# Kernel optimization log

Measured on AMD Instinct MI355X. Metric: run time of the kernel, lower is better.

## Reference

```python
import jax, jax.numpy as jnp
import numpy as np

H = 256; NHEAD = 2; DH = H // NHEAD; FF = NHEAD * H // 2
NODE_FEATS = [40, 8, 6]; EDGE_FEATS = [5, 4]; NIN = sum(NODE_FEATS)
S = 256; B = 4; NL_NODE = 2; NL_EDGE = 1
NEG = np.float32(-1e9)

# static edge-window bookkeeping: for i in 1..S-1, group i attends to nodes [max(0,i-12), i)
_idx = []; _grp = []
for _i in range(1, S):
    _st = max(0, _i - 12)
    _idx += list(range(_st, _i)); _grp += [_i] * (_i - _st)
IDX = np.asarray(_idx); GRP = np.asarray(_grp); LE = len(_idx)
MEM_MASK = np.full((LE, S + 1), NEG, np.float32)
MEM_MASK[:, 0] = 0.0; MEM_MASK[np.arange(LE), GRP + 1] = 0.0
EDGE_TGT_MASK = np.where(GRP[:, None] == GRP[None, :], np.float32(0.0), NEG)
CAUSAL = np.triu(np.full((S, S), NEG, np.float32), 1)
SIN_F = (1.0 / 10000.0 ** (np.arange(0, H, 2) / H)).astype(np.float32)
COS_F = (1.0 / 10000.0 ** (np.arange(1, H, 2) / H)).astype(np.float32)

def _ln(x, g, b):
    m = x.mean(-1, keepdims=True)
    v = ((x - m) ** 2).mean(-1, keepdims=True)
    return (x - m) / jnp.sqrt(v + 1e-5) * g + b

def _mha(q_in, kv_in, qkv_w, qkv_b, o_w, o_b, mask):
    Lq, Bb, _ = q_in.shape; Lk = kv_in.shape[0]
    wq, wk, wv = jnp.split(qkv_w, 3, 0); bq, bk, bv = jnp.split(qkv_b, 3, 0)
    q = (q_in @ wq.T + bq).reshape(Lq, Bb, NHEAD, DH)
    k = (kv_in @ wk.T + bk).reshape(Lk, Bb, NHEAD, DH)
    v = (kv_in @ wv.T + bv).reshape(Lk, Bb, NHEAD, DH)
    s = jnp.einsum('qbhd,kbhd->bhqk', q, k) * np.float32(1.0 / np.sqrt(DH))
    if mask is not None:
        s = s + mask
    p = jax.nn.softmax(s, -1)
    o = jnp.einsum('bhqk,kbhd->qbhd', p, v).reshape(Lq, Bb, H)
    return o @ o_w.T + o_b

def _decoder(tgt, mem, P, tgt_mask, mem_mask):
    qkv_w, qkv_b, so_w, so_b, cqkv_w, cqkv_b, co_w, co_b, f1w, f1b, f2w, f2b, lg, lb, fg, fb = P
    for l in range(qkv_w.shape[0]):
        tgt = _ln(tgt + _mha(tgt, tgt, qkv_w[l], qkv_b[l], so_w[l], so_b[l], tgt_mask), lg[l, 0], lb[l, 0])
        tgt = _ln(tgt + _mha(tgt, mem, cqkv_w[l], cqkv_b[l], co_w[l], co_b[l], mem_mask), lg[l, 1], lb[l, 1])
        ff = jax.nn.relu(tgt @ f1w[l].T + f1b[l]) @ f2w[l].T + f2b[l]
        tgt = _ln(tgt + ff, lg[l, 2], lb[l, 2])
    return _ln(tgt, fg, fb)

def _ce(logits, tgt):
    lp = jax.nn.log_softmax(logits, -1)
    nll = -jnp.take_along_axis(lp, jnp.clip(tgt, 0)[:, None], 1)[:, 0]
    valid = (tgt >= 0).astype(lp.dtype)
    return (nll * valid).sum() / jnp.maximum(valid.sum(), 1.0)

def _forward(z, atom_x, Wp, bp, bn_g, bn_b, ndP, edP, ncls, ecls, atom_i, atom_y, bond_y):
    x = atom_x.reshape(-1, NIN) @ Wp.T + bp
    m = x.mean(0); v2 = ((x - m) ** 2).mean(0)  # BatchNorm1d (training stats)
    x = jax.nn.selu((x - m) / jnp.sqrt(v2 + 1e-5) * bn_g + bn_b).reshape(S, B, H)
    pos = atom_i[..., 0].astype(jnp.float32)  # [S,B]
    pe = jnp.stack([jnp.sin(pos[:, :, None] * SIN_F), jnp.cos(pos[:, :, None] * COS_F)], -1).reshape(S, B, H)
    node_emb = _decoder(pe + x, z[None], ndP, CAUSAL, None)
    yt = atom_y.reshape(-1, atom_y.shape[-1])
    node_loss = 0.0
    for i, (w, b) in enumerate(ncls):
        node_loss = node_loss + _ce((node_emb @ w.T + b).reshape(-1, w.shape[0]), yt[:, i])
    edge_mem = jnp.concatenate([z[None], node_emb], 0)  # [S+1,B,H]
    edge_emb = _decoder(node_emb[IDX], edge_mem, edP, EDGE_TGT_MASK, MEM_MASK)
    et = bond_y.reshape(-1, bond_y.shape[-1])
    edge_loss = 0.0
    for i, (w, b) in enumerate(ecls):
        edge_loss = edge_loss + _ce((edge_emb @ w.T + b).reshape(-1, w.shape[0]), et[:, i])
    return node_loss + edge_loss

def setup_inputs():
    key = jax.random.key(0)
    cnt = [0]
    def nk():
        cnt[0] += 1
        return jax.random.fold_in(key, cnt[0])
    def rn(shape, s=0.05):
        return jax.random.normal(nk(), shape, jnp.float32) * s
    inp = {}
    inp['z'] = jax.random.normal(nk(), (B, H), jnp.float32)
    inp['atom_i'] = jax.random.randint(nk(), (S, B, 1), 0, S)
    inp['atom_x'] = jax.random.uniform(nk(), (S, B, NIN), dtype=jnp.float32)
    inp['atom_y'] = jax.random.randint(nk(), (S, B, 3), 0, 6)
    inp['bond_y'] = jax.random.randint(nk(), (LE, B, 2), 0, 4)
    inp['Wp'] = rn((H, NIN)); inp['bp'] = jnp.zeros((H,)); inp['bn_g'] = jnp.ones((H,)); inp['bn_b'] = jnp.zeros((H,))
    for pre, L in (('nd_', NL_NODE), ('ed_', NL_EDGE)):
        inp[pre + 'qkv_w'] = rn((L, 3 * H, H)); inp[pre + 'qkv_b'] = jnp.zeros((L, 3 * H))
        inp[pre + 'so_w'] = rn((L, H, H)); inp[pre + 'so_b'] = jnp.zeros((L, H))
        inp[pre + 'cqkv_w'] = rn((L, 3 * H, H)); inp[pre + 'cqkv_b'] = jnp.zeros((L, 3 * H))
        inp[pre + 'co_w'] = rn((L, H, H)); inp[pre + 'co_b'] = jnp.zeros((L, H))
        inp[pre + 'ff1_w'] = rn((L, FF, H)); inp[pre + 'ff1_b'] = jnp.zeros((L, FF))
        inp[pre + 'ff2_w'] = rn((L, H, FF)); inp[pre + 'ff2_b'] = jnp.zeros((L, H))
        inp[pre + 'ln_g'] = jnp.ones((L, 3, H)); inp[pre + 'ln_b'] = jnp.zeros((L, 3, H))
        inp[pre + 'fn_g'] = jnp.ones((H,)); inp[pre + 'fn_b'] = jnp.zeros((H,))
    for i, C in enumerate(NODE_FEATS):
        inp['nc%d_w' % i] = rn((C, H)); inp['nc%d_b' % i] = jnp.zeros((C,))
    for i, C in enumerate(EDGE_FEATS):
        inp['ec%d_w' % i] = rn((C, H)); inp['ec%d_b' % i] = jnp.zeros((C,))
    return inp

def reference(z, atom_i, atom_x, atom_y, bond_y, Wp, bp, bn_g, bn_b, nd_qkv_w, nd_qkv_b, nd_so_w, nd_so_b, nd_cqkv_w, nd_cqkv_b, nd_co_w, nd_co_b, nd_ff1_w, nd_ff1_b, nd_ff2_w, nd_ff2_b, nd_ln_g, nd_ln_b, nd_fn_g, nd_fn_b, ed_qkv_w, ed_qkv_b, ed_so_w, ed_so_b, ed_cqkv_w, ed_cqkv_b, ed_co_w, ed_co_b, ed_ff1_w, ed_ff1_b, ed_ff2_w, ed_ff2_b, ed_ln_g, ed_ln_b, ed_fn_g, ed_fn_b, nc0_w, nc0_b, nc1_w, nc1_b, nc2_w, nc2_b, ec0_w, ec0_b, ec1_w, ec1_b):
    ndP = (nd_qkv_w, nd_qkv_b, nd_so_w, nd_so_b, nd_cqkv_w, nd_cqkv_b, nd_co_w, nd_co_b, nd_ff1_w, nd_ff1_b, nd_ff2_w, nd_ff2_b, nd_ln_g, nd_ln_b, nd_fn_g, nd_fn_b)
    edP = (ed_qkv_w, ed_qkv_b, ed_so_w, ed_so_b, ed_cqkv_w, ed_cqkv_b, ed_co_w, ed_co_b, ed_ff1_w, ed_ff1_b, ed_ff2_w, ed_ff2_b, ed_ln_g, ed_ln_b, ed_fn_g, ed_fn_b)
    ncls = [(nc0_w, nc0_b), (nc1_w, nc1_b), (nc2_w, nc2_b)]
    ecls = [(ec0_w, ec0_b), (ec1_w, ec1_b)]
    return _forward(z, atom_x, Wp, bp, bn_g, bn_b, ndP, edP, ncls, ecls, atom_i, atom_y, bond_y)
```

## Files before the change

### kernel.cpp

```cpp
#include <hip/hip_runtime.h>
#include <math.h>

#define SS 256
#define BB 4
#define HH 256
#define LE 2994
#define LEB (LE*BB)
#define SCALE 0.08838834764831845f

typedef __attribute__((ext_vector_type(8))) short bf16x8;
typedef __attribute__((ext_vector_type(4))) float f32x4;

__device__ inline ushort f2b(float f) {
    unsigned u = __float_as_uint(f);
    u += 0x7FFFu + ((u >> 16) & 1u);
    return (ushort)(u >> 16);
}

__device__ inline float qred(float x) {
    x += __shfl_xor(x, 1); x += __shfl_xor(x, 2);
    x += __shfl_xor(x, 4); x += __shfl_xor(x, 8);
    return x;
}

// ... 232 lines not shown

__global__ __launch_bounds__(256) void k_node_mega(
    const float* __restrict__ t1, const float* __restrict__ tgt,
    const float* __restrict__ crO,
    const ushort* __restrict__ Wso, const float* __restrict__ so_b,
    const float* __restrict__ ln0g, const float* __restrict__ ln0b,
    const float* __restrict__ ln1g, const float* __restrict__ ln1b,
    const ushort* __restrict__ Wff1, const float* __restrict__ ff1_b,
    const ushort* __restrict__ Wff2, const float* __restrict__ ff2_b,
    const float* __restrict__ ln2g, const float* __restrict__ ln2b,
    const float* __restrict__ fng, const float* __restrict__ fnb,
    float* __restrict__ outp, int M, int finalln)
{
    __shared__ ushort As[8 * 512];
    __shared__ float red[128];
    int tid = threadIdx.x;
    int w = tid >> 6, lane = tid & 63, q = lane >> 4, p = lane & 15;
    int m0 = blockIdx.x * 16;

    float x[4][4];
    f32x4 acc[4];

    stageA_16(t1, M, m0, tid, As);
    #pragma unroll
    for (int reg = 0; reg < 4; reg++) {
        int row = m0 + q * 4 + reg;
        bool ok = row < M;
        #pragma unroll
        for (int nt = 0; nt < 4; nt++)
            x[nt][reg] = ok ? tgt[(size_t)row * 256 + w * 64 + nt * 16 + p] : 0.f;
    }

    gemm_pass16(As, Wso, w, lane, acc);
    {
        float bi[4];
        #pragma unroll
        for (int nt = 0; nt < 4; nt++) bi[nt] = so_b[w * 64 + nt * 16 + p];
        #pragma unroll
        for (int nt = 0; nt < 4; nt++)
            #pragma unroll
            for (int reg = 0; reg < 4; reg++)
                acc[nt][reg] += bi[nt] + x[nt][reg];
    }
    block_ln16(acc, red, tid, w, q, p, ln0g, ln0b);

    #pragma unroll
    for (int reg = 0; reg < 4; reg++) {
        int row = m0 + q * 4 + reg;
        int b = row & 3;
        #pragma unroll
        for (int nt = 0; nt < 4; nt++)
            acc[nt][reg] += crO[b * 256 + w * 64 + nt * 16 + p];
    }
    block_ln16(acc, red, tid, w, q, p, ln1g, ln1b);

    #pragma unroll
    for (int nt = 0; nt < 4; nt++)
        #pragma unroll
        for (int reg = 0; reg < 4; reg++)
            x[nt][reg] = acc[nt][reg];

    stage_acc16(acc, As, w, q, p);
    gemm_pass16(As, Wff1, w, lane, acc);
    {
        float bi[4];
        #pragma unroll
        for (int nt = 0; nt < 4; nt++) bi[nt] = ff1_b[w * 64 + nt * 16 + p];
        #pragma unroll
        for (int nt = 0; nt < 4; nt++)
            #pragma unroll
            for (int reg = 0; reg < 4; reg++)
                acc[nt][reg] = fmaxf(acc[nt][reg] + bi[nt], 0.f);
    }

    stage_acc16(acc, As, w, q, p);
    gemm_pass16(As, Wff2, w, lane, acc);
    {
        float bi[4];
        #pragma unroll
        for (int nt = 0; nt < 4; nt++) bi[nt] = ff2_b[w * 64 + nt * 16 + p];
        #pragma unroll
        for (int nt = 0; nt < 4; nt++)
            #pragma unroll
            for (int reg = 0; reg < 4; reg++)
                acc[nt][reg] += bi[nt] + x[nt][reg];
    }
    block_ln16(acc, red, tid, w, q, p, ln2g, ln2b);
    if (finalln) block_ln16(acc, red, tid, w, q, p, fng, fnb);

    #pragma unroll
    for (int reg = 0; reg < 4; reg++) {
        int row = m0 + q * 4 + reg;
        if (row >= M) continue;
        #pragma unroll
        for (int nt = 0; nt < 4; nt++)
            outp[(size_t)row * 256 + w * 64 + nt * 16 + p] = acc[nt][reg];
    }
}


__global__ __launch_bounds__(256) void k_edge_mega(
    const float* __restrict__ et1, const float* __restrict__ etgt,
    const ushort* __restrict__ Wso, const float* __restrict__ so_b,
    const float* __restrict__ ln0g, const float* __restrict__ ln0b,
    const ushort* __restrict__ Wcq, const float* __restrict__ cq_b,
    const float* __restrict__ KV, const int* __restrict__ grp,
    const ushort* __restrict__ Wco, const float* __restrict__ co_b,
    const float* __restrict__ ln1g, const float* __restrict__ ln1b,
    const ushort* __restrict__ Wff1, const float* __restrict__ ff1_b,
    const ushort* __restrict__ Wff2, const float* __restrict__ ff2_b,
    const float* __restrict__ ln2g, const float* __restrict__ ln2b,
    const float* __restrict__ fng, const float* __restrict__ fnb,
    const int* __restrict__ ydata,
    const float* __restrict__ cw0, const float* __restrict__ cb0,
    const float* __restrict__ cw1, const float* __restrict__ cb1,
    float* __restrict__ lossOut, float invM, int M)
{
    __shared__ ushort As[8 * 512];
    __shared__ float red[640];
    int tid = threadIdx.x;
    int w = tid >> 6, lane = tid & 63, q = lane >> 4, p = lane & 15;
    int m0 = blockIdx.x * 16;

    float x[4][4];
    f32x4 acc[4];

    stageA_16(et1, M, m0, tid, As);
    #pragma unroll
    for (int reg = 0; reg < 4; reg++) {
        int row = m0 + q * 4 + reg;
        bool ok = row < M;
        #pragma unroll
        for (int nt = 0; nt < 4; nt++)
            x[nt][reg] = ok ? etgt[(size_t)row * 256 + w * 64 + nt * 16 + p] : 0.f;
    }

    gemm_pass16(As, Wso, w, lane, acc);
    {
        float bi[4];
        #pragma unroll
        for (int nt = 0; nt < 4; nt++) bi[nt] = so_b[w * 64 + nt * 16 + p];
        #pragma unroll
        for (int nt = 0; nt < 4; nt++)
            #pragma unroll
            for (int reg = 0; reg < 4; reg++)
                acc[nt][reg] += bi[nt] + x[nt][reg];
    }
    block_ln16(acc, red, tid, w, q, p, ln0g, ln0b);
    #pragma unroll
    for (int nt = 0; nt < 4; nt++)
        #pragma unroll
        for (int reg = 0; reg < 4; reg++)
            x[nt][reg] = acc[nt][reg];

    stage_acc16(acc, As, w, q, p);
    gemm_pass16(As, Wcq, w, lane, acc);
    {
        int h = w >> 1;
        float bi[4];
        #pragma unroll
        for (int nt = 0; nt < 4; nt++) bi[nt] = cq_b[w * 64 + nt * 16 + p];
        #pragma unroll
        for (int reg = 0; reg < 4; reg++) {
            int lr = q * 4 + reg;
            int row = m0 + lr;
            bool ok = row < M;
            int b = row & 3;
            int g = ok ? grp[row >> 2] : 0;
            const float* K0 = KV + (size_t)b * 512 + h * 128;
            const float* K1 = KV + ((size_t)(g + 1) * 4 + b) * 512 + h * 128;
            float s0 = 0.f, s1 = 0.f;
            #pragma unroll
            for (int nt = 0; nt < 4; nt++) {
                float qv = acc[nt][reg] + bi[nt];
                int d = (w & 1) * 64 + nt * 16 + p;
                s0 += qv * K0[d]; s1 += qv * K1[d];
            }
            s0 = qred(s0); s1 = qred(s1);
            if (p == 0) { red[(w * 16 + lr) * 2 + 0] = s0; red[(w * 16 + lr) * 2 + 1] = s1; }
        }
        __syncthreads();
        if (tid < 32) {
            int hh = tid >> 4, lr = tid & 15;
            float p0 = (red[((hh * 2) * 16 + lr) * 2 + 0] + red[((hh * 2 + 1) * 16 + lr) * 2 + 0]) * SCALE;
            float p1 = (red[((hh * 2) * 16 + lr) * 2 + 1] + red[((hh * 2 + 1) * 16 + lr) * 2 + 1]) * SCALE;
            float mx = fmaxf(p0, p1);
            float e0 = __expf(p0 - mx), e1 = __expf(p1 - mx);
            float inv = 1.f / (e0 + e1);
            red[128 + (hh * 16 + lr) * 2 + 0] = e0 * inv;
            red[128 + (hh * 16 + lr) * 2 + 1] = e1 * inv;
        }
        __syncthreads();
        #pragma unroll
        for (int reg = 0; reg < 4; reg++) {
            int lr = q * 4 + reg;
            int row = m0 + lr;
            bool ok = row < M;
            int b = row & 3;
            int g = ok ? grp[row >> 2] : 0;
            float e0 = red[128 + (h * 16 + lr) * 2 + 0];
            float e1 = red[128 + (h * 16 + lr) * 2 + 1];
            const float* V0 = KV + (size_t)b * 512 + 256 + h * 128;
            const float* V1 = KV + ((size_t)(g + 1) * 4 + b) * 512 + 256 + h * 128;
            #pragma unroll
            for (int nt = 0; nt < 4; nt++) {
                int d = (w & 1) * 64 + nt * 16 + p;
                acc[nt][reg] = e0 * V0[d] + e1 * V1[d];
            }
        }
        __syncthreads();
    }

    stage_acc16(acc, As, w, q, p);
    gemm_pass16(As, Wco, w, lane, acc);
    {
        float bi[4];
        #pragma unroll
        for (int nt = 0; nt < 4; nt++) bi[nt] = co_b[w * 64 + nt * 16 + p];
        #pragma unroll
        for (int nt = 0; nt < 4; nt++)
            #pragma unroll
            for (int reg = 0; reg < 4; reg++)
                acc[nt][reg] += bi[nt] + x[nt][reg];
    }
    block_ln16(acc, red, tid, w, q, p, ln1g, ln1b);
    #pragma unroll
    for (int nt = 0; nt < 4; nt++)
        #pragma unroll
        for (int reg = 0; reg < 4; reg++)
            x[nt][reg] = acc[nt][reg];

    stage_acc16(acc, As, w, q, p);
    gemm_pass16(As, Wff1, w, lane, acc);
    {
        float bi[4];
        #pragma unroll
        for (int nt = 0; nt < 4; nt++) bi[nt] = ff1_b[w * 64 + nt * 16 + p];
        #pragma unroll
        for (int nt = 0; nt < 4; nt++)
            #pragma unroll
            for (int reg = 0; reg < 4; reg++)
                acc[nt][reg] = fmaxf(acc[nt][reg] + bi[nt], 0.f);
    }

    stage_acc16(acc, As, w, q, p);
    gemm_pass16(As, Wff2, w, lane, acc);
    {
        float bi[4];
        #pragma unroll
        for (int nt = 0; nt < 4; nt++) bi[nt] = ff2_b[w * 64 + nt * 16 + p];
        #pragma unroll
        for (int nt = 0; nt < 4; nt++)
            #pragma unroll
            for (int reg = 0; reg < 4; reg++)
                acc[nt][reg] += bi[nt] + x[nt][reg];
    }
    block_ln16(acc, red, tid, w, q, p, ln2g, ln2b);
    block_ln16(acc, red, tid, w, q, p, fng, fnb);

    #pragma unroll
    for (int c = 0; c < 9; c++) {
        const float* wc = (c < 5) ? (cw0 + (size_t)c * 256) : (cw1 + (size_t)(c - 5) * 256);
        float wv[4];
        #pragma unroll
        for (int nt = 0; nt < 4; nt++) wv[nt] = wc[w * 64 + nt * 16 + p];
        #pragma unroll
        for (int reg = 0; reg < 4; reg++) {
            float s = acc[0][reg] * wv[0] + acc[1][reg] * wv[1]
                    + acc[2][reg] * wv[2] + acc[3][reg] * wv[3];
            s = qred(s);
            if (p == 0) red[(c * 4 + w) * 16 + q * 4 + reg] = s;
        }
    }
    __syncthreads();
    if (tid < 16) {
        float local = 0.f;
        int grow = m0 + tid;
        if (grow < M) {
            int y0 = ydata[(size_t)grow * 2 + 0], y1 = ydata[(size_t)grow * 2 + 1];
            float lg[9];
            #pragma unroll
            for (int c = 0; c < 9; c++)
                lg[c] = red[(c * 4 + 0) * 16 + tid] + red[(c * 4 + 1) * 16 + tid]
                      + red[(c * 4 + 2) * 16 + tid] + red[(c * 4 + 3) * 16 + tid]
                      + ((c < 5) ? cb0[c] : cb1[c - 5]);
            float mA = -1e30f, mB = -1e30f, tA = 0.f, tB = 0.f;
            #pragma unroll
            for (int c = 0; c < 5; c++) { mA = fmaxf(mA, lg[c]); if (c == y0) tA = lg[c]; }
            #pragma unroll
            for (int c = 0; c < 4; c++) { mB = fmaxf(mB, lg[5 + c]); if (c == y1) tB = lg[5 + c]; }
            float sA = 0.f, sB = 0.f;
            #pragma unroll
            for (int c = 0; c < 5; c++) sA += __expf(lg[c] - mA);
            #pragma unroll
            for (int c = 0; c < 4; c++) sB += __expf(lg[5 + c] - mB);
            local = (mA + logf(sA) - tA) + (mB + logf(sB) - tB);
        }
        for (int o = 8; o; o >>= 1) local += __shfl_down(local, o);
        if (tid == 0) atomicAdd(lossOut, local * invM);
    }
}


__global__ __launch_bounds__(256) void k_attn_qks(
    const float* __restrict__ qkv, ushort* __restrict__ P)
{
    __shared__ ushort Qs[64 * 32];
    __shared__ ushort Ks[256 * 32];
    int tid = threadIdx.x;
    int wave = tid >> 6, lane = tid & 63;
    int q = lane >> 4, p = lane & 15;
    int m0 = blockIdx.x * 64;
    int z = blockIdx.y, b = z >> 1, h = z & 1;
    size_t qoff = (size_t)b * 768 + h * 128;

    f32x4 acc[16];
    #pragma unroll
    for (int i = 0; i < 16; i++) acc[i] = (f32x4){0.f, 0.f, 0.f, 0.f};

    int sra = tid >> 2, sca = (tid & 3) << 3;
    const float* Arow = qkv + (size_t)(m0 + sra) * 3072 + qoff + sca;
    const float* Wrow = qkv + (size_t)tid * 3072 + qoff + 256;
    ushort* asd = &Qs[sra * 32 + sca];
    ushort* wsd = &Ks[tid * 32];

    for (int k0 = 0; k0 < 128; k0 += 32) {
        float4 a0 = *(const float4*)(Arow + k0);
        float4 a1 = *(const float4*)(Arow + k0 + 4);
        float av[8] = {a0.x, a0.y, a0.z, a0.w, a1.x, a1.y, a1.z, a1.w};
        float wv[32];
        #pragma unroll
        for (int i = 0; i < 8; i++) {
            float4 w4 = *(const float4*)(Wrow + k0 + i * 4);
            wv[i*4+0] = w4.x; wv[i*4+1] = w4.y; wv[i*4+2] = w4.z; wv[i*4+3] = w4.w;
        }
        unsigned au[4], wu[16];
        #pragma unroll
        for (int i = 0; i < 4; i++) au[i] = (unsigned)f2b(av[2*i]) | ((unsigned)f2b(av[2*i+1]) << 16);
        #pragma unroll
        for (int i = 0; i < 16; i++) wu[i] = (unsigned)f2b(wv[2*i]) | ((unsigned)f2b(wv[2*i+1]) << 16);
        __syncthreads();
        ((uint4*)asd)[0] = make_uint4(au[0], au[1], au[2], au[3]);
        ((uint4*)wsd)[0] = make_uint4(wu[0], wu[1], wu[2], wu[3]);
        ((uint4*)(wsd + 8))[0] = make_uint4(wu[4], wu[5], wu[6], wu[7]);
        ((uint4*)(wsd + 16))[0] = make_uint4(wu[8], wu[9], wu[10], wu[11]);
        ((uint4*)(wsd + 24))[0] = make_uint4(wu[12], wu[13], wu[14], wu[15]);
        __syncthreads();

        bf16x8 af = *(const bf16x8*)&Qs[(wave * 16 + p) * 32 + q * 8];
        #pragma unroll
        for (int nt = 0; nt < 16; nt++) {
            bf16x8 bf = *(const bf16x8*)&Ks[(nt * 16 + p) * 32 + q * 8];
            acc[nt] = __builtin_amdgcn_mfma_f32_16x16x32_bf16(af, bf, acc[nt], 0, 0, 0);
        }
    }

    ushort* Pz = P + (size_t)z * 65536;
    #pragma unroll
    for (int reg = 0; reg < 4; reg++) {
        int row = m0 + wave * 16 + q * 4 + reg;
        float v[16]; float mx = -1e30f;
        #pragma unroll
        for (int nt = 0; nt < 16; nt++) {
            int colk = nt * 16 + p;
            float val = (colk <= row) ? acc[nt][reg] * SCALE : -1e30f;
            v[nt] = val; mx = fmaxf(mx, val);
        }
        mx = fmaxf(mx, __shfl_xor(mx, 1)); mx = fmaxf(mx, __shfl_xor(mx, 2));
        mx = fmaxf(mx, __shfl_xor(mx, 4)); mx = fmaxf(mx, __shfl_xor(mx, 8));
        float s = 0.f;
        #pragma unroll
        for (int nt = 0; nt < 16; nt++) {
            int colk = nt * 16 + p;
            float e = (colk <= row) ? __expf(v[nt] - mx) : 0.f;
            v[nt] = e; s += e;
        }
        s += __shfl_xor(s, 1); s += __shfl_xor(s, 2); s += __shfl_xor(s, 4); s += __shfl_xor(s, 8);
        float inv = 1.f / s;
        #pragma unroll
        for (int nt = 0; nt < 16; nt++)
            Pz[(size_t)row * 256 + nt * 16 + p] = f2b(v[nt] * inv);
    }
}


__global__ __launch_bounds__(256) void k_attn_pvt(
    const ushort* __restrict__ P, const float* __restrict__ Vt,
    float* __restrict__ out)
{
    __shared__ ushort As[64 * 32];
    __shared__ ushort Bs[128 * 32];
    int tid = threadIdx.x;
    int wave = tid >> 6, lane = tid & 63;
    int q = lane >> 4, p = lane & 15;
    int m0 = blockIdx.x * 64;
    int z = blockIdx.y, b = z >> 1, h = z & 1;

    f32x4 acc[8];
    #pragma unroll
    for (int i = 0; i < 8; i++) acc[i] = (f32x4){0.f, 0.f, 0.f, 0.f};

    int sra = tid >> 2, sca = (tid & 3) << 3;
    const ushort* Prow = P + (size_t)z * 65536 + (size_t)(m0 + sra) * 256 + sca;
    int srb = tid >> 1, scb = (tid & 1) << 4;
    const float* Vrow = Vt + (size_t)z * 32768 + (size_t)srb * 256 + scb;
    ushort* asd = &As[sra * 32 + sca];
    ushort* wsd = &Bs[srb * 32 + scb];

    for (int k0 = 0; k0 < 256; k0 += 32) {
        uint4 pa = *(const uint4*)(Prow + k0);
        float wv[16];
        #pragma unroll
        for (int i = 0; i < 4; i++) {
            float4 w4 = *(const float4*)(Vrow + k0 + i * 4);
            wv[i*4+0] = w4.x; wv[i*4+1] = w4.y; wv[i*4+2] = w4.z; wv[i*4+3] = w4.w;
        }
        unsigned wu[8];
        #pragma unroll
        for (int i = 0; i < 8; i++) wu[i] = (unsigned)f2b(wv[2*i]) | ((unsigned)f2b(wv[2*i+1]) << 16);
        __syncthreads();
        ((uint4*)asd)[0] = pa;
        ((uint4*)wsd)[0] = make_uint4(wu[0], wu[1], wu[2], wu[3]);
        ((uint4*)(wsd + 8))[0] = make_uint4(wu[4], wu[5], wu[6], wu[7]);
        __syncthreads();

        bf16x8 af = *(const bf16x8*)&As[(wave * 16 + p) * 32 + q * 8];
        #pragma unroll
        for (int nt = 0; nt < 8; nt++) {
            bf16x8 bf = *(const bf16x8*)&Bs[(nt * 16 + p) * 32 + q * 8];
            acc[nt] = __builtin_amdgcn_mfma_f32_16x16x32_bf16(af, bf, acc[nt], 0, 0, 0);
        }
    }

    #pragma unroll
    for (int reg = 0; reg < 4; reg++) {
        int s = m0 + wave * 16 + q * 4 + reg;
        #pragma unroll
        for (int nt = 0; nt < 8; nt++) {
            int dh = nt * 16 + p;
            out[(size_t)s * 1024 + (size_t)b * 256 + h * 128 + dh] = acc[nt][reg];
        }
    }
}


__global__ __launch_bounds__(256) void k_gemm(
    const float* __restrict__ A, const float* __restrict__ W,
    const float* __restrict__ bias, float* __restrict__ C,
    int M, int N, int K, int relu)
{
    __shared__ __align__(16) float As[16][68];
    __shared__ __align__(16) float Ws[16][68];
    int tx = threadIdx.x, ty = threadIdx.y;
    int tid = ty * 16 + tx;
    int m0 = blockIdx.y * 64, n0 = blockIdx.x * 64;
    float acc[4][4] = {{0.f}};
    int r  = tid >> 2;
    int kk = (tid & 3) << 2;
    for (int k0 = 0; k0 < K; k0 += 16) {
        float4 av = make_float4(0.f, 0.f, 0.f, 0.f);
        float4 wv = make_float4(0.f, 0.f, 0.f, 0.f);
        int gm = m0 + r, gk = k0 + kk;
        if (gm < M) {
            float tv[4];
            for (int i = 0; i < 4; i++) tv[i] = (gk + i < K) ? A[(size_t)gm * K + gk + i] : 0.f;
            av = make_float4(tv[0], tv[1], tv[2], tv[3]);
        }
        int gn = n0 + r;
        if (gn < N) {
            float tv[4];
            for (int i = 0; i < 4; i++) tv[i] = (gk + i < K) ? W[(size_t)gn * K + gk + i] : 0.f;
            wv = make_float4(tv[0], tv[1], tv[2], tv[3]);
        }
        As[kk + 0][r] = av.x; As[kk + 1][r] = av.y; As[kk + 2][r] = av.z; As[kk + 3][r] = av.w;
        Ws[kk + 0][r] = wv.x; Ws[kk + 1][r] = wv.y; Ws[kk + 2][r] = wv.z; Ws[kk + 3][r] = wv.w;
        __syncthreads();
        #pragma unroll
        for (int k = 0; k < 16; k++) {
            float4 a4 = *(const float4*)&As[k][ty << 2];
            float4 b4 = *(const float4*)&Ws[k][tx << 2];
            float a[4] = {a4.x, a4.y, a4.z, a4.w};
            float b[4] = {b4.x, b4.y, b4.z, b4.w};
            #pragma unroll
            for (int i = 0; i < 4; i++)
                #pragma unroll
                for (int j = 0; j < 4; j++)
                    acc[i][j] = fmaf(a[i], b[j], acc[i][j]);
        }
        __syncthreads();
    }
    #pragma unroll
    for (int i = 0; i < 4; i++) {
        int gm = m0 + (ty << 2) + i;
        if (gm >= M) continue;
        #pragma unroll
        for (int j = 0; j < 4; j++) {
            int gn = n0 + (tx << 2) + j;
            if (gn >= N) continue;
            float v = acc[i][j] + bias[gn];
            if (relu) v = fmaxf(v, 0.f);
            C[(size_t)gm * N + gn] = v;
        }
    }
}


__global__ __launch_bounds__(256) void k_bn_part(const float* __restrict__ x, float* __restrict__ sums) {
    int t = threadIdx.x;
    int r0 = blockIdx.x * 16;
    float s = 0.f, s2 = 0.f;
    for (int r = r0; r < r0 + 16; r++) {
        float v = x[(size_t)r * 256 + t];
        s += v; s2 += v * v;
    }
    atomicAdd(&sums[t], s);
    atomicAdd(&sums[256 + t], s2);
}


__global__ __launch_bounds__(256) void k_bn_selu_pe(
    const float* __restrict__ x0, const float* __restrict__ sums,
    const float* __restrict__ g, const float* __restrict__ b,
    const int* __restrict__ atom_i, float* __restrict__ out)
{
    int row = blockIdx.x, t = threadIdx.x;
    float m = sums[t] * (1.f / 1024.f);
    float var = sums[256 + t] * (1.f / 1024.f) - m * m;
    float rstd = rsqrtf(var + 1e-5f);
    float v = x0[(size_t)row * 256 + t];
    v = (v - m) * rstd * g[t] + b[t];
    const float SC = 1.0507009873554805f, AL = 1.6732632423543772f;
    v = SC * (v > 0.f ? v : AL * expm1f(v));
    float pos = (float)atom_i[row];
    float freq = expf(-(float)t * (9.210340371976184f / 256.f));
    float ang = pos * freq;
    float pe = (t & 1) ? cosf(ang) : sinf(ang);
    out[(size_t)row * 256 + t] = v + pe;
}


__global__ __launch_bounds__(256) void k_cross2(
    const float* __restrict__ z, const float* __restrict__ cqkv_w, const float* __restrict__ cqkv_b,
    const float* __restrict__ co_w, const float* __restrict__ co_b, float* __restrict__ crO)
{
    int m = blockIdx.x, l = blockIdx.y;
    int t = threadIdx.x;
    __shared__ float zs[256], ct[256];
    zs[t] = z[m * 256 + t];
    __syncthreads();
    const float* wv = cqkv_w + (size_t)l * 768 * 256 + 512 * 256 + (size_t)t * 256;
    float a = cqkv_b[l * 768 + 512 + t];
    for (int d = 0; d < 256; d += 4) {
        float4 w4 = *(const float4*)(wv + d);
        a += zs[d] * w4.x + zs[d+1] * w4.y + zs[d+2] * w4.z + zs[d+3] * w4.w;
    }
    ct[t] = a;
    __syncthreads();
    const float* ow = co_w + (size_t)l * 65536 + (size_t)t * 256;
    float o = co_b[l * 256 + t];
    for (int d = 0; d < 256; d += 4) {
        float4 w4 = *(const float4*)(ow + d);
        o += ct[d] * w4.x + ct[d+1] * w4.y + ct[d+2] * w4.z + ct[d+3] * w4.w;
    }
    crO[l * 1024 + m * 256 + t] = o;
}


__global__ __launch_bounds__(256) void k_edge_self_attn(
    const float* __restrict__ qkv, float* __restrict__ out)
{
    int g = blockIdx.x + 1;
    int b = blockIdx.y;
    int gs = min(g, 12);
    int base = (g <= 13) ? g * (g - 1) / 2 : 78 + (g - 13) * 12;
    int h = threadIdx.x >> 7;
    int t = threadIdx.x & 127;
    __shared__ float qs[2][12][128], ks[2][12][128], vs[2][12][128];
    __shared__ float ps[2][12][12];
    for (int i = 0; i < gs; i++) {
        size_t row = ((size_t)(base + i) * BB + b) * 768 + h * 128 + t;
        qs[h][i][t] = qkv[row];
        ks[h][i][t] = qkv[row + 256];
        vs[h][i][t] = qkv[row + 512];
    }
    __syncthreads();
    for (int p = t; p < gs * gs; p += 128) {
        int i = p / gs, j = p - i * gs;
        float acc = 0.f;
        for (int d = 0; d < 128; d++) acc = fmaf(qs[h][i][d], ks[h][j][d], acc);
        ps[h][i][j] = acc * SCALE;
    }
    __syncthreads();
    if (t < gs) {
        float m = -1e30f;
        for (int j = 0; j < gs; j++) m = fmaxf(m, ps[h][t][j]);
        float e[12]; float s = 0.f;
        for (int j = 0; j < gs; j++) { e[j] = expf(ps[h][t][j] - m); s += e[j]; }
        float inv = 1.f / s;
        for (int j = 0; j < gs; j++) ps[h][t][j] = e[j] * inv;
    }
    __syncthreads();
    for (int i = 0; i < gs; i++) {
        float acc = 0.f;
        for (int j = 0; j < gs; j++) acc = fmaf(ps[h][i][j], vs[h][j][t], acc);
        out[((size_t)(base + i) * BB + b) * 256 + h * 128 + t] = acc;
    }
}


__global__ __launch_bounds__(256) void k_gather_mem(
    const float* __restrict__ z, const float* __restrict__ nemb,
    const int* __restrict__ idxt, float* __restrict__ etgt, float* __restrict__ memb)
{
    int r = blockIdx.x, t = threadIdx.x;
    if (r < LEB) {
        int e = r >> 2, b = r & 3;
        etgt[(size_t)r * 256 + t] = nemb[((size_t)idxt[e] * 4 + b) * 256 + t];
    } else {
        int rm = r - LEB;
        int m = rm >> 2, b = rm & 3;
        memb[(size_t)rm * 256 + t] = (m == 0) ? z[(size_t)b * 256 + t]
                                              : nemb[((size_t)(m - 1) * 4 + b) * 256 + t];
    }
}


__global__ __launch_bounds__(256) void k_ce_node(
    const float* __restrict__ emb,
    const float* __restrict__ w0, const float* __restrict__ b0,
    const float* __restrict__ w1, const float* __restrict__ b1,
    const float* __restrict__ w2, const float* __restrict__ b2,
    const int* __restrict__ y, int M, float invM, float* __restrict__ lossOut)
{
    int wave = threadIdx.x >> 6, lane = threadIdx.x & 63;
    int wid = blockIdx.x * 4 + wave;
    float local = 0.f;
    for (int r = wid; r < M; r += gridDim.x * 4) {
        float4 x = ((const float4*)(emb + (size_t)r * 256))[lane];
        float acc[54];
        #pragma unroll
        for (int c = 0; c < 40; c++) {
            float4 wv = ((const float4*)(w0 + (size_t)c * 256))[lane];
            acc[c] = x.x * wv.x + x.y * wv.y + x.z * wv.z + x.w * wv.w;
        }
        #pragma unroll
        for (int c = 0; c < 8; c++) {
            float4 wv = ((const float4*)(w1 + (size_t)c * 256))[lane];
            acc[40 + c] = x.x * wv.x + x.y * wv.y + x.z * wv.z + x.w * wv.w;
        }
        #pragma unroll
        for (int c = 0; c < 6; c++) {
            float4 wv = ((const float4*)(w2 + (size_t)c * 256))[lane];
            acc[48 + c] = x.x * wv.x + x.y * wv.y + x.z * wv.z + x.w * wv.w;
        }
        #pragma unroll
        for (int c = 0; c < 54; c++)
            for (int o = 32; o; o >>= 1) acc[c] += __shfl_down(acc[c], o);
        if (lane == 0) {
            int y0 = y[(size_t)r * 3 + 0], y1 = y[(size_t)r * 3 + 1], y2 = y[(size_t)r * 3 + 2];
            float m0v = -1e30f, m1v = -1e30f, m2v = -1e30f;
            float t0 = 0.f, t1v = 0.f, t2v = 0.f;
            #pragma unroll
            for (int c = 0; c < 40; c++) {
                float v = acc[c] + b0[c];
                acc[c] = v; m0v = fmaxf(m0v, v);
                if (c == y0) t0 = v;
            }
            #pragma unroll
            for (int c = 0; c < 8; c++) {
                float v = acc[40 + c] + b1[c];
                acc[40 + c] = v; m1v = fmaxf(m1v, v);
                if (c == y1) t1v = v;
            }
            #pragma unroll
            for (int c = 0; c < 6; c++) {
                float v = acc[48 + c] + b2[c];
                acc[48 + c] = v; m2v = fmaxf(m2v, v);
                if (c == y2) t2v = v;
            }
            float s0 = 0.f, s1 = 0.f, s2 = 0.f;
            #pragma unroll
            for (int c = 0; c < 40; c++) s0 += __expf(acc[c] - m0v);
            #pragma unroll
            for (int c = 0; c < 8; c++)  s1 += __expf(acc[40 + c] - m1v);
            #pragma unroll
            for (int c = 0; c < 6; c++)  s2 += __expf(acc[48 + c] - m2v);
            local += (m0v + logf(s0) - t0) + (m1v + logf(s1) - t1v) + (m2v + logf(s2) - t2v);
        }
    }
    __shared__ float ls[4];
    if (lane == 0) ls[wave] = local;
    __syncthreads();
    if (threadIdx.x == 0)
        atomicAdd(lossOut, (ls[0] + ls[1] + ls[2] + ls[3]) * invM);
}


extern "C" void kernel_launch(void* const* d_in, const int* in_sizes, int n_in,
                              void* d_out, int out_size, void* d_ws, size_t ws_size,
                              hipStream_t stream)
{
    (void)in_sizes; (void)n_in; (void)out_size; (void)ws_size;
    const float* zin      = (const float*)d_in[0];
    const int*   atom_i   = (const int*)d_in[1];
    const float* atom_x   = (const float*)d_in[2];
    const int*   atom_y   = (const int*)d_in[3];
    const int*   bond_y   = (const int*)d_in[4];
    const float* Wp       = (const float*)d_in[5];
    const float* bp       = (const float*)d_in[6];
    const float* bn_g     = (const float*)d_in[7];
    const float* bn_b     = (const float*)d_in[8];
    const float* nd_qkv_w = (const float*)d_in[9];
    const float* nd_qkv_b = (const float*)d_in[10];
    const float* nd_so_w  = (const float*)d_in[11];
    const float* nd_so_b  = (const float*)d_in[12];
    const float* nd_cqkv_w= (const float*)d_in[13];
    const float* nd_cqkv_b= (const float*)d_in[14];
    const float* nd_co_w  = (const float*)d_in[15];
    const float* nd_co_b  = (const float*)d_in[16];
    const float* nd_ff1_w = (const float*)d_in[17];
    const float* nd_ff1_b = (const float*)d_in[18];
    const float* nd_ff2_w = (const float*)d_in[19];
    const float* nd_ff2_b = (const float*)d_in[20];
    const float* nd_ln_g  = (const float*)d_in[21];
    const float* nd_ln_b  = (const float*)d_in[22];
    const float* nd_fn_g  = (const float*)d_in[23];
    const float* nd_fn_b  = (const float*)d_in[24];
    const float* ed_qkv_w = (const float*)d_in[25];
    const float* ed_qkv_b = (const float*)d_in[26];
    const float* ed_so_w  = (const float*)d_in[27];
    const float* ed_so_b  = (const float*)d_in[28];
    const float* ed_cqkv_w= (const float*)d_in[29];
    const float* ed_cqkv_b= (const float*)d_in[30];
    const float* ed_co_w  = (const float*)d_in[31];
    const float* ed_co_b  = (const float*)d_in[32];
    const float* ed_ff1_w = (const float*)d_in[33];
    const float* ed_ff1_b = (const float*)d_in[34];
    const float* ed_ff2_w = (const float*)d_in[35];
    const float* ed_ff2_b = (const float*)d_in[36];
    const float* ed_ln_g  = (const float*)d_in[37];
    const float* ed_ln_b  = (const float*)d_in[38];
    const float* ed_fn_g  = (const float*)d_in[39];
    const float* ed_fn_b  = (const float*)d_in[40];
    const float* nc0_w = (const float*)d_in[41]; const float* nc0_b = (const float*)d_in[42];
    const float* nc1_w = (const float*)d_in[43]; const float* nc1_b = (const float*)d_in[44];
    const float* nc2_w = (const float*)d_in[45]; const float* nc2_b = (const float*)d_in[46];
    const float* ec0_w = (const float*)d_in[47]; const float* ec0_b = (const float*)d_in[48];
    const float* ec1_w = (const float*)d_in[49]; const float* ec1_b = (const float*)d_in[50];

    float* out = (float*)d_out;

    char* wsb = (char*)d_ws;
    size_t off = 0;
    auto alloc = [&](size_t nbytes) -> void* {
        void* p = (void*)(wsb + off);
        off += (nbytes + 255) / 256 * 256;
        return p;
    };
    float* x0    = (float*)alloc(1024 * 256 * 4);
    float* tgt   = (float*)alloc(1024 * 256 * 4);
    float* nqkv  = (float*)alloc(1024 * 768 * 4);
    float* t1    = (float*)alloc(1024 * 256 * 4);
    float* nemb  = (float*)alloc(1024 * 256 * 4);
    float* bnsums= (float*)alloc(512 * 4);
    float* crO   = (float*)alloc(2 * 1024 * 4);
    float* memb  = (float*)alloc(1028 * 256 * 4);
    float* KV    = (float*)alloc(1028 * 512 * 4);
    ushort* Sb   = (ushort*)alloc(8 * 65536 * 2);
    float* Vt    = (float*)alloc(8 * 32768 * 4);
    float* etgt  = (float*)alloc((size_t)LEB * 256 * 4);
    float* eqkv  = (float*)alloc((size_t)LEB * 768 * 4);
    float* et1   = (float*)alloc((size_t)LEB * 256 * 4);
    int* grp   = (int*)alloc(LE * 4);
    int* idxt  = (int*)alloc(LE * 4);
    ushort* wpk = (ushort*)alloc((size_t)TOTFRAG * 512 * 2);

    PackArgs pa;
    pa.src[0] = nd_qkv_w;              pa.src[1] = nd_qkv_w + 768 * 256;
    pa.src[2] = nd_so_w;               pa.src[3] = nd_so_w + 65536;
    pa.src[4] = nd_ff1_w;              pa.src[5] = nd_ff1_w + 65536;
    pa.src[6] = nd_ff2_w;              pa.src[7] = nd_ff2_w + 65536;
    pa.src[8] = ed_qkv_w;              pa.src[9] = ed_cqkv_w;
    pa.src[10] = ed_so_w;              pa.src[11] = ed_co_w;
    pa.src[12] = ed_ff1_w;             pa.src[13] = ed_ff2_w;
    int fs[NPACK + 1] = {0, 384, 768, 896, 1024, 1152, 1280, 1408, 1536, 1920, 2304, 2432, 2560, 2688, 2816};
    for (int i = 0; i <= NPACK; i++) pa.fs[i] = fs[i];
    auto wp = [&](int i) -> const ushort* { return wpk + (size_t)fs[i] * 512; };

    k_init<<<13, 256, 0, stream>>>(out, bnsums, grp, idxt);
    k_prep<<<(TOTFRAG * 64 + 255) / 256, 256, 0, stream>>>(pa, wpk);

    k_gemm<<<dim3(4, 16), dim3(16, 16), 0, stream>>>(atom_x, Wp, bp, x0, 1024, 256, 54, 0);
    k_bn_part<<<64, 256, 0, stream>>>(x0, bnsums);
    k_bn_selu_pe<<<1024, 256, 0, stream>>>(x0, bnsums, bn_g, bn_b, atom_i, tgt);

    k_cross2<<<dim3(4, 2), 256, 0, stream>>>(zin, nd_cqkv_w, nd_cqkv_b, nd_co_w, nd_co_b, crO);

    for (int l = 0; l < 2; l++) {
        k_gemm_w<<<dim3(3, 8), 256, 0, stream>>>(tgt, wp(l), nd_qkv_b + l * 768,
                                                 nqkv, Vt, 1024, 768, 3, 0);
        k_attn_qks<<<dim3(4, 8), 256, 0, stream>>>(nqkv, Sb);
        k_attn_pvt<<<dim3(4, 8), 256, 0, stream>>>(Sb, Vt, t1);
        k_node_mega<<<64, 256, 0, stream>>>(
            t1, tgt, crO + l * 1024,
            wp(2 + l), nd_so_b + l * 256,
            nd_ln_g + (l * 3 + 0) * 256, nd_ln_b + (l * 3 + 0) * 256,
            nd_ln_g + (l * 3 + 1) * 256, nd_ln_b + (l * 3 + 1) * 256,
            wp(4 + l), nd_ff1_b + l * 256,
            wp(6 + l), nd_ff2_b + l * 256,
            nd_ln_g + (l * 3 + 2) * 256, nd_ln_b + (l * 3 + 2) * 256,
            nd_fn_g, nd_fn_b,
            (l == 0) ? tgt : nemb, 1024, (l == 1) ? 1 : 0);
    }

    k_ce_node<<<128, 256, 0, stream>>>(nemb, nc0_w, nc0_b, nc1_w, nc1_b, nc2_w, nc2_b,
                                       atom_y, 1024, 1.f / 1024.f, out);

    k_gather_mem<<<LEB + 1028, 256, 0, stream>>>(zin, nemb, idxt, etgt, memb);
    k_gemm_w<<<dim3(2, 17), 256, 0, stream>>>(memb, wp(9) + 128 * 512, ed_cqkv_b + 256,
                                              KV, nullptr, 1028, 512, 0, 0);
    k_gemm_w<<<dim3(3, 188), 256, 0, stream>>>(etgt, wp(8), ed_qkv_b,
                                               eqkv, nullptr, LEB, 768, 0, 0);
    k_edge_self_attn<<<dim3(255, 4), 256, 0, stream>>>(eqkv, et1);
    k_edge_mega<<<(LEB + 15) / 16, 256, 0, stream>>>(
        et1, etgt,
        wp(10), ed_so_b, ed_ln_g, ed_ln_b,
        wp(9), ed_cqkv_b, KV, grp,
        wp(11), ed_co_b, ed_ln_g + 256, ed_ln_b + 256,
        wp(12), ed_ff1_b,
        wp(13), ed_ff2_b, ed_ln_g + 512, ed_ln_b + 512,
        ed_fn_g, ed_fn_b,
        bond_y, ec0_w, ec0_b, ec1_w, ec1_b,
        out, 1.f / (float)LEB, LEB);
}
```

Measured before the change: 452.0 us.

## Fuse node attention score and PV kernels; fuse edge QKV projection into edge attention

The node self-attention score/softmax kernel now keeps the bf16 probability tile in shared memory and performs the P·V MFMA in the same kernel, reading V directly from global memory and converting it per fragment. This removes the round trip of the probability matrix through global memory and one launch. The edge path fuses the QKV projection GEMM into the per-group windowed attention kernel, so the large eqkv intermediate is never written or re-read. The cost is more shared memory per block, un-staged V loads with redundant conversion, and a 16-row MFMA tile of which at most 12 rows are used per group.

```diff
diff --git a/kernel.cpp b/kernel.cpp
--- a/kernel.cpp
+++ b/kernel.cpp
@@ -558,11 +558,13 @@
 }
 
 
-__global__ __launch_bounds__(256) void k_attn_qks(
-    const float* __restrict__ qkv, ushort* __restrict__ P)
+__global__ __launch_bounds__(256) void k_attn_fused(
+    const float* __restrict__ qkv, const float* __restrict__ Vt,
+    float* __restrict__ outp)
 {
     __shared__ ushort Qs[64 * 32];
     __shared__ ushort Ks[256 * 32];
+    __shared__ ushort Pl[32 * 512];
     int tid = threadIdx.x;
     int wave = tid >> 6, lane = tid & 63;
     int q = lane >> 4, p = lane & 15;
@@ -611,7 +613,6 @@
         }
     }
 
-    ushort* Pz = P + (size_t)z * 65536;
     #pragma unroll
     for (int reg = 0; reg < 4; reg++) {
         int row = m0 + wave * 16 + q * 4 + reg;
@@ -635,67 +636,120 @@
         float inv = 1.f / s;
         #pragma unroll
         for (int nt = 0; nt < 16; nt++)
-            Pz[(size_t)row * 256 + nt * 16 + p] = f2b(v[nt] * inv);
-    }
-}
-
-
-__global__ __launch_bounds__(256) void k_attn_pvt(
-    const ushort* __restrict__ P, const float* __restrict__ Vt,
-    float* __restrict__ out)
+            Pl[(wave * 8 + (nt >> 1)) * 512 +
+               ((((nt * 2) + (p >> 3)) & 3) * 16 + q * 4 + reg) * 8 + (p & 7)] = f2b(v[nt] * inv);
+    }
+
+    f32x4 a2[8];
+    #pragma unroll
+    for (int i = 0; i < 8; i++) a2[i] = (f32x4){0.f, 0.f, 0.f, 0.f};
+    #pragma unroll
+    for (int kt = 0; kt < 8; kt++) {
+        bf16x8 af = *(const bf16x8*)&Pl[(wave * 8 + kt) * 512 + lane * 8];
+        #pragma unroll
+        for (int nt = 0; nt < 8; nt++) {
+            const float* vr = Vt + (size_t)z * 32768 + (size_t)(nt * 16 + p) * 256 + kt * 32 + q * 8;
+            float4 v0 = *(const float4*)vr;
+            float4 v1 = *(const float4*)(vr + 4);
+            uint4 wu = make_uint4(f2b(v0.x) | ((unsigned)f2b(v0.y) << 16),
+                                  f2b(v0.z) | ((unsigned)f2b(v0.w) << 16),
+                                  f2b(v1.x) | ((unsigned)f2b(v1.y) << 16),
+                                  f2b(v1.z) | ((unsigned)f2b(v1.w) << 16));
+            bf16x8 bf = *(bf16x8*)&wu;
+            a2[nt] = __builtin_amdgcn_mfma_f32_16x16x32_bf16(af, bf, a2[nt], 0, 0, 0);
+        }
+    }
+    #pragma unroll
+    for (int reg = 0; reg < 4; reg++) {
+        int row = m0 + wave * 16 + q * 4 + reg;
+        #pragma unroll
+        for (int nt = 0; nt < 8; nt++)
+            outp[(size_t)row * 1024 + (size_t)b * 256 + h * 128 + nt * 16 + p] = a2[nt][reg];
+    }
+}
+
+
+__global__ __launch_bounds__(256) void k_edge_qkv_attn(
+    const float* __restrict__ etgt, const ushort* __restrict__ Wq,
+    const float* __restrict__ bias, float* __restrict__ et1)
 {
-    __shared__ ushort As[64 * 32];
-    __shared__ ushort Bs[128 * 32];
+    __shared__ ushort As[8 * 512];
+    __shared__ float qlds[12 * 768];
+    __shared__ float ps[2][12][12];
     int tid = threadIdx.x;
-    int wave = tid >> 6, lane = tid & 63;
-    int q = lane >> 4, p = lane & 15;
-    int m0 = blockIdx.x * 64;
-    int z = blockIdx.y, b = z >> 1, h = z & 1;
-
-    f32x4 acc[8];
-    #pragma unroll
-    for (int i = 0; i < 8; i++) acc[i] = (f32x4){0.f, 0.f, 0.f, 0.f};
-
-    int sra = tid >> 2, sca = (tid & 3) << 3;
-    const ushort* Prow = P + (size_t)z * 65536 + (size_t)(m0 + sra) * 256 + sca;
-    int srb = tid >> 1, scb = (tid & 1) << 4;
-    const float* Vrow = Vt + (size_t)z * 32768 + (size_t)srb * 256 + scb;
-    ushort* asd = &As[sra * 32 + sca];
-    ushort* wsd = &Bs[srb * 32 + scb];
-
-    for (int k0 = 0; k0 < 256; k0 += 32) {
-        uint4 pa = *(const uint4*)(Prow + k0);
-        float wv[16];
-        #pragma unroll
-        for (int i = 0; i < 4; i++) {
-            float4 w4 = *(const float4*)(Vrow + k0 + i * 4);
-            wv[i*4+0] = w4.x; wv[i*4+1] = w4.y; wv[i*4+2] = w4.z; wv[i*4+3] = w4.w;
-        }
-        unsigned wu[8];
-        #pragma unroll
-        for (int i = 0; i < 8; i++) wu[i] = (unsigned)f2b(wv[2*i]) | ((unsigned)f2b(wv[2*i+1]) << 16);
-        __syncthreads();
-        ((uint4*)asd)[0] = pa;
-        ((uint4*)wsd)[0] = make_uint4(wu[0], wu[1], wu[2], wu[3]);
-        ((uint4*)(wsd + 8))[0] = make_uint4(wu[4], wu[5], wu[6], wu[7]);
-        __syncthreads();
-
-        bf16x8 af = *(const bf16x8*)&As[(wave * 16 + p) * 32 + q * 8];
-        #pragma unroll
-        for (int nt = 0; nt < 8; nt++) {
-            bf16x8 bf = *(const bf16x8*)&Bs[(nt * 16 + p) * 32 + q * 8];
-            acc[nt] = __builtin_amdgcn_mfma_f32_16x16x32_bf16(af, bf, acc[nt], 0, 0, 0);
-        }
-    }
-
-    #pragma unroll
-    for (int reg = 0; reg < 4; reg++) {
-        int s = m0 + wave * 16 + q * 4 + reg;
-        #pragma unroll
-        for (int nt = 0; nt < 8; nt++) {
-            int dh = nt * 16 + p;
-            out[(size_t)s * 1024 + (size_t)b * 256 + h * 128 + dh] = acc[nt][reg];
-        }
+    int w = tid >> 6, lane = tid & 63, q = lane >> 4, p = lane & 15;
+    int g = blockIdx.x + 1;
+    int b = blockIdx.y;
+    int gs = min(g, 12);
+    int base = (g <= 13) ? g * (g - 1) / 2 : 78 + (g - 13) * 12;
+
+    {
+        int r = tid >> 4;
+        int cbase = (tid & 15) * 16;
+        bool ok = r < gs;
+        const float* Ar = etgt + ((size_t)(base + r) * 4 + b) * 256 + cbase;
+        #pragma unroll
+        for (int j = 0; j < 2; j++) {
+            int c = cbase + j * 8;
+            float4 a0, a1;
+            if (ok) { a0 = *(const float4*)(Ar + j * 8); a1 = *(const float4*)(Ar + j * 8 + 4); }
+            else { a0 = make_float4(0.f, 0.f, 0.f, 0.f); a1 = a0; }
+            uint4 o = make_uint4(f2b(a0.x) | ((unsigned)f2b(a0.y) << 16),
+                                 f2b(a0.z) | ((unsigned)f2b(a0.w) << 16),
+                                 f2b(a1.x) | ((unsigned)f2b(a1.y) << 16),
+                                 f2b(a1.z) | ((unsigned)f2b(a1.w) << 16));
+            *(uint4*)&As[(c >> 5) * 512 + (((c >> 3) & 3) * 16 + r) * 8] = o;
+        }
+    }
+    __syncthreads();
+
+    f32x4 acc[12];
+    #pragma unroll
+    for (int j = 0; j < 12; j++) acc[j] = (f32x4){0.f, 0.f, 0.f, 0.f};
+    #pragma unroll
+    for (int kt = 0; kt < 8; kt++) {
+        bf16x8 af = *(const bf16x8*)&As[kt * 512 + lane * 8];
+        #pragma unroll
+        for (int j = 0; j < 12; j++) {
+            bf16x8 wf = *(const bf16x8*)&Wq[(size_t)((w * 12 + j) * 8 + kt) * 512 + lane * 8];
+            acc[j] = __builtin_amdgcn_mfma_f32_16x16x32_bf16(af, wf, acc[j], 0, 0, 0);
+        }
+    }
+    #pragma unroll
+    for (int j = 0; j < 12; j++) {
+        int col = (w * 12 + j) * 16 + p;
+        float bi = bias[col];
+        #pragma unroll
+        for (int reg = 0; reg < 4; reg++) {
+            int row = q * 4 + reg;
+            if (row < 12) qlds[row * 768 + col] = acc[j][reg] + bi;
+        }
+    }
+    __syncthreads();
+
+    int h = tid >> 7, t = tid & 127;
+    for (int pidx = t; pidx < gs * gs; pidx += 128) {
+        int i = pidx / gs, jj = pidx - i * gs;
+        const float* qp = &qlds[i * 768 + h * 128];
+        const float* kp = &qlds[jj * 768 + 256 + h * 128];
+        float a = 0.f;
+        for (int d = 0; d < 128; d++) a = fmaf(qp[d], kp[d], a);
+        ps[h][i][jj] = a * SCALE;
+    }
+    __syncthreads();
+    if (t < gs) {
+        float m = -1e30f;
+        for (int jj = 0; jj < gs; jj++) m = fmaxf(m, ps[h][t][jj]);
+        float e[12]; float s = 0.f;
+        for (int jj = 0; jj < gs; jj++) { e[jj] = __expf(ps[h][t][jj] - m); s += e[jj]; }
+        float inv = 1.f / s;
+        for (int jj = 0; jj < gs; jj++) ps[h][t][jj] = e[jj] * inv;
+    }
+    __syncthreads();
+    for (int i = 0; i < gs; i++) {
+        float a = 0.f;
+        for (int jj = 0; jj < gs; jj++) a = fmaf(ps[h][i][jj], qlds[jj * 768 + 512 + h * 128 + t], a);
+        et1[((size_t)(base + i) * 4 + b) * 256 + h * 128 + t] = a;
     }
 }
 
@@ -819,48 +873,6 @@
         o += ct[d] * w4.x + ct[d+1] * w4.y + ct[d+2] * w4.z + ct[d+3] * w4.w;
     }
     crO[l * 1024 + m * 256 + t] = o;
-}
-
-
-__global__ __launch_bounds__(256) void k_edge_self_attn(
-    const float* __restrict__ qkv, float* __restrict__ out)
-{
-    int g = blockIdx.x + 1;
-    int b = blockIdx.y;
-    int gs = min(g, 12);
-    int base = (g <= 13) ? g * (g - 1) / 2 : 78 + (g - 13) * 12;
-    int h = threadIdx.x >> 7;
-    int t = threadIdx.x & 127;
-    __shared__ float qs[2][12][128], ks[2][12][128], vs[2][12][128];
-    __shared__ float ps[2][12][12];
-    for (int i = 0; i < gs; i++) {
-        size_t row = ((size_t)(base + i) * BB + b) * 768 + h * 128 + t;
-        qs[h][i][t] = qkv[row];
-        ks[h][i][t] = qkv[row + 256];
-        vs[h][i][t] = qkv[row + 512];
-    }
-    __syncthreads();
-    for (int p = t; p < gs * gs; p += 128) {
-        int i = p / gs, j = p - i * gs;
-        float acc = 0.f;
-        for (int d = 0; d < 128; d++) acc = fmaf(qs[h][i][d], ks[h][j][d], acc);
-        ps[h][i][j] = acc * SCALE;
-    }
-    __syncthreads();
-    if (t < gs) {
-        float m = -1e30f;
-        for (int j = 0; j < gs; j++) m = fmaxf(m, ps[h][t][j]);
-        float e[12]; float s = 0.f;
-        for (int j = 0; j < gs; j++) { e[j] = expf(ps[h][t][j] - m); s += e[j]; }
-        float inv = 1.f / s;
-        for (int j = 0; j < gs; j++) ps[h][t][j] = e[j] * inv;
-    }
-    __syncthreads();
-    for (int i = 0; i < gs; i++) {
-        float acc = 0.f;
-        for (int j = 0; j < gs; j++) acc = fmaf(ps[h][i][j], vs[h][j][t], acc);
-        out[((size_t)(base + i) * BB + b) * 256 + h * 128 + t] = acc;
-    }
 }
 
 
@@ -1022,10 +1034,8 @@
     float* crO   = (float*)alloc(2 * 1024 * 4);
     float* memb  = (float*)alloc(1028 * 256 * 4);
     float* KV    = (float*)alloc(1028 * 512 * 4);
-    ushort* Sb   = (ushort*)alloc(8 * 65536 * 2);
     float* Vt    = (float*)alloc(8 * 32768 * 4);
     float* etgt  = (float*)alloc((size_t)LEB * 256 * 4);
-    float* eqkv  = (float*)alloc((size_t)LEB * 768 * 4);
     float* et1   = (float*)alloc((size_t)LEB * 256 * 4);
     int* grp   = (int*)alloc(LE * 4);
     int* idxt  = (int*)alloc(LE * 4);
@@ -1055,8 +1065,7 @@
     for (int l = 0; l < 2; l++) {
         k_gemm_w<<<dim3(3, 8), 256, 0, stream>>>(tgt, wp(l), nd_qkv_b + l * 768,
                                                  nqkv, Vt, 1024, 768, 3, 0);
-        k_attn_qks<<<dim3(4, 8), 256, 0, stream>>>(nqkv, Sb);
-        k_attn_pvt<<<dim3(4, 8), 256, 0, stream>>>(Sb, Vt, t1);
+        k_attn_fused<<<dim3(4, 8), 256, 0, stream>>>(nqkv, Vt, t1);
         k_node_mega<<<64, 256, 0, stream>>>(
             t1, tgt, crO + l * 1024,
             wp(2 + l), nd_so_b + l * 256,
@@ -1075,9 +1084,7 @@
     k_gather_mem<<<LEB + 1028, 256, 0, stream>>>(zin, nemb, idxt, etgt, memb);
     k_gemm_w<<<dim3(2, 17), 256, 0, stream>>>(memb, wp(9) + 128 * 512, ed_cqkv_b + 256,
                                               KV, nullptr, 1028, 512, 0, 0);
-    k_gemm_w<<<dim3(3, 188), 256, 0, stream>>>(etgt, wp(8), ed_qkv_b,
-                                               eqkv, nullptr, LEB, 768, 0, 0);
-    k_edge_self_attn<<<dim3(255, 4), 256, 0, stream>>>(eqkv, et1);
+    k_edge_qkv_attn<<<dim3(255, 4), 256, 0, stream>>>(etgt, wp(8), ed_qkv_b, et1);
     k_edge_mega<<<(LEB + 15) / 16, 256, 0, stream>>>(
         et1, etgt,
         wp(10), ed_so_b, ed_ln_g, ed_ln_b,
```

Result: no change. 453.7 us (+0.4%).
